# Kernel tuning notes

Hardware: AMD Instinct MI355X
Metric: run time of the kernel (lower is better)

## Reference

```python
import jax, jax.numpy as jnp
import numpy as np

N_NODES = 50000
N_EDGES = 1600000
IN_DIM = 128
OUT_DIM = 32
N_HEADS = 4


def setup_inputs() -> dict:
    key = jax.random.key(0)
    k_x, k_e, k_w, k_a = jax.random.split(key, 4)
    x = jax.random.normal(k_x, (N_NODES, IN_DIM), dtype=jnp.float32)
    edge_index = jax.random.randint(k_e, (N_EDGES, 2), 0, N_NODES, dtype=jnp.int64)
    # Xavier-uniform-like init scales
    w_bound = np.sqrt(6.0 / (IN_DIM + OUT_DIM)).astype(np.float32)
    a_bound = np.sqrt(6.0 / (N_HEADS + 2 * OUT_DIM)).astype(np.float32)
    weight = jax.random.uniform(k_w, (N_HEADS, IN_DIM, OUT_DIM), dtype=jnp.float32,
                                minval=-w_bound, maxval=w_bound)
    attn = jax.random.uniform(k_a, (N_HEADS, 2 * OUT_DIM), dtype=jnp.float32,
                              minval=-a_bound, maxval=a_bound)
    return {"x": x, "edge_index": edge_index, "weight": weight, "attn": attn}


def reference(x, edge_index, weight, attn):
    # x: [N, in_dim]; edge_index: [E, 2]; weight: [H, in, out]; attn: [H, 2*out]
    num_nodes = x.shape[0]
    out_dim = weight.shape[2]
    src = edge_index[:, 0]
    dst = edge_index[:, 1]

    # Per-head linear transform: [N, H, out]
    Wh = jnp.einsum('ni,hio->nho', x, weight)
    Wh_src = Wh[src]  # [E, H, out]
    Wh_dst = Wh[dst]  # [E, H, out]

    a_src = attn[:, :out_dim]   # [H, out]
    a_dst = attn[:, out_dim:]   # [H, out]
    # Edge scores: [E, H]
    e = jnp.einsum('eho,ho->eh', Wh_src, a_src) + jnp.einsum('eho,ho->eh', Wh_dst, a_dst)
    e = jax.nn.leaky_relu(e, negative_slope=0.2)

    # Segment softmax over incoming edges of each dst node
    max_per_dst = jax.ops.segment_max(e, dst, num_segments=num_nodes)  # [N, H]
    max_per_dst = jnp.where(jnp.isfinite(max_per_dst), max_per_dst, 0.0)
    exp_e = jnp.exp(e - max_per_dst[dst])                               # [E, H]
    sum_per_dst = jax.ops.segment_sum(exp_e, dst, num_segments=num_nodes)  # [N, H]
    alpha = exp_e / (sum_per_dst[dst] + 1e-9)                           # [E, H]
    # Dropout is identity in eval mode.

    # Weighted scatter-add aggregation: [N, H, out]
    out = jax.ops.segment_sum(alpha[:, :, None] * Wh_src, dst, num_segments=num_nodes)
    h = out.reshape(num_nodes, -1)  # concat heads -> [N, H*out]
    return h, alpha
```

## Files before the change

### kernel.cpp

```cpp
#include <hip/hip_runtime.h>
#include <hip/hip_bf16.h>
#include <math.h>

#define N_NODES 50000
#define N_EDGES 1600000
#define IN_DIM  128
#define OUT_DIM 32
#define N_HEADS 4
#define WH_DIM  (N_HEADS * OUT_DIM)
#define CAP     128
#define NB_SCAN 196
#define NPASS   4
#define WIN     (N_NODES / NPASS)
#define NCHUNK  32
#define CE      (N_EDGES / NCHUNK)

typedef __attribute__((ext_vector_type(8))) short short8;
typedef __attribute__((ext_vector_type(4))) float floatx4;

__device__ __forceinline__ short f2bf(float v) {
    __hip_bfloat16 b = __float2bfloat16(v);
    return *reinterpret_cast<short*>(&b);
}
__device__ __forceinline__ float lrelu(float v) {
    return v > 0.0f ? v : 0.2f * v;
}

__device__ __forceinline__ void load_edge(const void* eidx, int is32, int e,
                                          int& s, int& d) {
    if (is32) {
        const int2 v = ((const int2*)eidx)[e];
        s = v.x; d = v.y;
    } else {
        const longlong2 v = ((const longlong2*)eidx)[e];
        s = (int)v.x; d = (int)v.y;
    }
}

__global__ void k_detect(const int* __restrict__ eidx, int* __restrict__ flag) {
    int i = threadIdx.x;
    int r = eidx[2 * (i * (N_EDGES / 256)) + 1];
    if (r != 0) atomicOr(flag, 1);
}

__global__ __launch_bounds__(256) void k_cvt(
        const void* __restrict__ eidx, const int* __restrict__ flag,
        int* __restrict__ s32, int* __restrict__ d32) {
    int e = blockIdx.x * 256 + threadIdx.x;
    if (e >= N_EDGES) return;
    int s, d;
    load_edge(eidx, *flag, e, s, d);
    s32[e] = s;
    d32[e] = d;
}

__global__ __launch_bounds__(256) void k_wh(
        const float* __restrict__ x, const float* __restrict__ weight,
        const float* __restrict__ attn,
        __hip_bfloat16* __restrict__ Wh16, float* __restrict__ sb16) {
    __shared__ float ubuf[128 * 8];
    __shared__ short xsw[4 * 4 * 64 * 8];
    __shared__ short bsw[4 * 9 * 64 * 8];
    const int t  = threadIdx.x;
    const int nb = blockIdx.x * 64;

    {
        int c = t & 7, k0 = t >> 3;
        int h = c & 3;
        const float* ap = attn + h * 64 + (c >> 2) * 32;
        for (int k = k0; k < 128; k += 32) {
            const float* wp = weight + h * (IN_DIM * OUT_DIM) + k * OUT_DIM;
            float u = 0.f;
#pragma unroll
            for (int o = 0; o < 32; o += 4) {
                float4 wv = *(const float4*)(wp + o);
                float4 av = *(const float4*)(ap + o);
                u += wv.x * av.x + wv.y * av.y + wv.z * av.z + wv.w * av.w;
            }
            ubuf[k * 8 + c] = u;
        }
    }
    __syncthreads();

    for (int f = t; f < 128 * 128; f += 256) {
        int k = f >> 7, c = f & 127;
        float w = weight[(c >> 5) * (IN_DIM * OUT_DIM) + k * OUT_DIM + (c & 31)];
        int kc = k >> 5, quad = (k >> 3) & 3, j = k & 7;
        bsw[((kc * 9 + (c >> 4)) * 64 + quad * 16 + (c & 15)) * 8 + j] = f2bf(w);
    }
    for (int f = t; f < 128 * 16; f += 256) {
        int k = f >> 4, c = f & 15;
        float w = (c < 8) ? ubuf[k * 8 + c] : 0.f;
        int kc = k >> 5, quad = (k >> 3) & 3, j = k & 7;
        bsw[((kc * 9 + 8) * 64 + quad * 16 + c) * 8 + j] = f2bf(w);
    }
    for (int f = t; f < 64 * 32; f += 256) {
        int n = f >> 5, k = (f & 31) * 4;
        int ng = nb + n; if (ng > N_NODES - 1) ng = N_NODES - 1;
        float4 v = *(const float4*)(x + (size_t)ng * IN_DIM + k);
        int wg = n >> 4, m = n & 15, kc = k >> 5, quad = (k >> 3) & 3, j = k & 7;
        short4 sv = make_short4(f2bf(v.x), f2bf(v.y), f2bf(v.z), f2bf(v.w));
        *(short4*)&xsw[(((wg * 4 + kc) * 64) + quad * 16 + m) * 8 + j] = sv;
    }
    __syncthreads();

    const int wg = t >> 6, lane = t & 63;
    floatx4 acc[9];
#pragma unroll
    for (int i = 0; i < 9; ++i) acc[i] = (floatx4){0.f, 0.f, 0.f, 0.f};
#pragma unroll
    for (int kc = 0; kc < 4; ++kc) {
        short8 a = *(short8*)&xsw[((wg * 4 + kc) * 64 + lane) * 8];
#pragma unroll
        for (int cg = 0; cg < 9; ++cg) {
            short8 b = *(short8*)&bsw[((kc * 9 + cg) * 64 + lane) * 8];
            acc[cg] = __builtin_amdgcn_mfma_f32_16x16x32_bf16(a, b, acc[cg],
                                                              0, 0, 0);
        }
    }

    const int col = lane & 15, quad = lane >> 4;
#pragma unroll
    for (int r = 0; r < 4; ++r) {
        int n = nb + wg * 16 + quad * 4 + r;
        if (n >= N_NODES) continue;
#pragma unroll
        for (int cg = 0; cg < 8; ++cg)
            Wh16[(size_t)n * WH_DIM + cg * 16 + col] =
                __float2bfloat16(acc[cg][r]);
        if (col < 8) sb16[(size_t)n * 16 + col] = acc[8][r];
    }
}

__global__ __launch_bounds__(1024) void k_hist(
        const int* __restrict__ d32, int* __restrict__ hist) {
    __shared__ int hbin[WIN];
    const int c = blockIdx.x, w = blockIdx.y;
    for (int i = threadIdx.x; i < WIN; i += 1024) hbin[i] = 0;
    __syncthreads();
    const int w0 = w * WIN;
    for (int e = c * CE + threadIdx.x; e < (c + 1) * CE; e += 1024) {
        unsigned u = (unsigned)(d32[e] - w0);
        if (u < WIN) atomicAdd(&hbin[u], 1);
    }
    __syncthreads();
    for (int i = threadIdx.x; i < WIN; i += 1024)
        hist[c * N_NODES + w0 + i] = hbin[i];
}

__global__ __launch_bounds__(256) void k_scan1(
        const int* __restrict__ hist, int* __restrict__ pre,
        int* __restrict__ bsum) {
    __shared__ int sh[256];
    const int t = threadIdx.x;
    const int i = blockIdx.x * 256 + t;
    int v = 0;
    if (i < N_NODES)
        for (int c = 0; c < NCHUNK; ++c) v += hist[c * N_NODES + i];
    sh[t] = v;
    __syncthreads();
    for (int d = 1; d < 256; d <<= 1) {
        int u = (t >= d) ? sh[t - d] : 0;
        __syncthreads();
        sh[t] += u;
        __syncthreads();
    }
    if (i < N_NODES) pre[i] = sh[t] - v;
    if (t == 255) bsum[blockIdx.x] = sh[255];
}

__global__ __launch_bounds__(256) void k_scan2(
        const int* __restrict__ bsum, int* __restrict__ bbase) {
    __shared__ int sh[256];
    const int t = threadIdx.x;
    int v = (t < NB_SCAN) ? bsum[t] : 0;
    sh[t] = v;
    __syncthreads();
    for (int d = 1; d < 256; d <<= 1) {
        int u = (t >= d) ? sh[t - d] : 0;
        __syncthreads();
        sh[t] += u;
        __syncthreads();
    }
    if (t < NB_SCAN) bbase[t] = sh[t] - v;
}

__global__ __launch_bounds__(256) void k_base(
        const int* __restrict__ pre, const int* __restrict__ bbase,
        int* __restrict__ hist) {
    int d = blockIdx.x * 256 + threadIdx.x;
    if (d >= N_NODES) return;
    int run = pre[d] + bbase[d >> 8];
    for (int c = 0; c < NCHUNK; ++c) {
        int t0 = hist[c * N_NODES + d];
        hist[c * N_NODES + d] = run;
        run += t0;
    }
}

__global__ __launch_bounds__(1024) void k_scatter(
        const int* __restrict__ s32, const int* __restrict__ d32,
        const int* __restrict__ hist, int* __restrict__ csr) {
    __shared__ int pos[WIN];
    const int c = blockIdx.x, w = blockIdx.y;
    const int w0 = w * WIN;
    for (int i = threadIdx.x; i < WIN; i += 1024)
        pos[i] = hist[c * N_NODES + w0 + i];
    __syncthreads();
    for (int e = c * CE + threadIdx.x; e < (c + 1) * CE; e += 1024) {
        unsigned u = (unsigned)(d32[e] - w0);
        if (u < WIN) {
            int p = atomicAdd(&pos[u], 1);
            csr[p] = s32[e];
        }
    }
}

__global__ __launch_bounds__(256) void k_node(
        const int* __restrict__ pre, const int* __restrict__ bbase,
        const int* __restrict__ csr, float* __restrict__ sb16,
        const __hip_bfloat16* __restrict__ Wh16,
        float* __restrict__ out_h) {
    __shared__ int    sbuf[4][CAP];
    __shared__ float4 e4b[4][CAP];
    const int wv = threadIdx.x >> 6;
    const int t  = threadIdx.x & 63;
    const int n  = blockIdx.x * 4 + wv;
    const int beg = pre[n] + bbase[n >> 8];
    const int end = (n + 1 < N_NODES) ? pre[n + 1] + bbase[(n + 1) >> 8]
                                      : N_EDGES;
    const int deg = end - beg;

    const float4 sd = *(const float4*)(sb16 + (size_t)n * 16 + 4);

    float4 sum = {0.f, 0.f, 0.f, 0.f};
    for (int l = t; l < deg; l += 64) {
        int s = csr[beg + l];
        float4 ss = *(const float4*)(sb16 + (size_t)s * 16);
        float4 ex;
        ex.x = __expf(lrelu(ss.x + sd.x));
        ex.y = __expf(lrelu(ss.y + sd.y));
        ex.z = __expf(lrelu(ss.z + sd.z));
        ex.w = __expf(lrelu(ss.w + sd.w));
        if (l < CAP) { sbuf[wv][l] = s; e4b[wv][l] = ex; }
        sum.x += ex.x; sum.y += ex.y; sum.z += ex.z; sum.w += ex.w;
    }
#pragma unroll
    for (int o = 32; o; o >>= 1) {
        sum.x += __shfl_xor(sum.x, o);
        sum.y += __shfl_xor(sum.y, o);
        sum.z += __shfl_xor(sum.z, o);
        sum.w += __shfl_xor(sum.w, o);
    }
    float4 inv;
    inv.x = 1.0f / (sum.x + 1e-9f); inv.y = 1.0f / (sum.y + 1e-9f);
    inv.z = 1.0f / (sum.z + 1e-9f); inv.w = 1.0f / (sum.w + 1e-9f);
    if (t == 0) *(float4*)(sb16 + (size_t)n * 16 + 8) = inv;

    const int h = t >> 4;
    const float invh = (h == 0) ? inv.x : (h == 1) ? inv.y
                     : (h == 2) ? inv.z : inv.w;
    float2 acc = {0.0f, 0.0f};
    if (deg <= CAP) {
        int j = 0;
        for (; j + 3 < deg; j += 4) {
            int s0 = sbuf[wv][j],     s1 = sbuf[wv][j + 1];
            int s2 = sbuf[wv][j + 2], s3 = sbuf[wv][j + 3];
            float a0 = ((const float*)&e4b[wv][j])[h]     * invh;
            float a1 = ((const float*)&e4b[wv][j + 1])[h] * invh;
            float a2 = ((const float*)&e4b[wv][j + 2])[h] * invh;
            float a3 = ((const float*)&e4b[wv][j + 3])[h] * invh;
            __hip_bfloat162 w0 = ((const __hip_bfloat162*)(Wh16 + (size_t)s0 * WH_DIM))[t];
            __hip_bfloat162 w1 = ((const __hip_bfloat162*)(Wh16 + (size_t)s1 * WH_DIM))[t];
            __hip_bfloat162 w2 = ((const __hip_bfloat162*)(Wh16 + (size_t)s2 * WH_DIM))[t];
            __hip_bfloat162 w3 = ((const __hip_bfloat162*)(Wh16 + (size_t)s3 * WH_DIM))[t];
            float2 f0 = __bfloat1622float2(w0);
            float2 f1 = __bfloat1622float2(w1);
            float2 f2 = __bfloat1622float2(w2);
            float2 f3 = __bfloat1622float2(w3);
            acc.x += a0 * f0.x + a1 * f1.x + a2 * f2.x + a3 * f3.x;
            acc.y += a0 * f0.y + a1 * f1.y + a2 * f2.y + a3 * f3.y;
        }
        for (; j < deg; ++j) {
            int s0 = sbuf[wv][j];
            float a0 = ((const float*)&e4b[wv][j])[h] * invh;
            __hip_bfloat162 w0 = ((const __hip_bfloat162*)(Wh16 + (size_t)s0 * WH_DIM))[t];
            float2 f0 = __bfloat1622float2(w0);
            acc.x += a0 * f0.x;
            acc.y += a0 * f0.y;
        }
    } else {
        float dh = (h == 0) ? sd.x : (h == 1) ? sd.y : (h == 2) ? sd.z : sd.w;
        for (int j = 0; j < deg; ++j) {
            int s0; float a0;
            if (j < CAP) {
                s0 = sbuf[wv][j];
                a0 = ((const float*)&e4b[wv][j])[h] * invh;
            } else {
                s0 = csr[beg + j];
                float sh = sb16[(size_t)s0 * 16 + h];
                a0 = __expf(lrelu(sh + dh)) * invh;
            }
            __hip_bfloat162 w0 = ((const __hip_bfloat162*)(Wh16 + (size_t)s0 * WH_DIM))[t];
            float2 f0 = __bfloat1622float2(w0);
            acc.x += a0 * f0.x;
            acc.y += a0 * f0.y;
        }
    }
    *(float2*)(out_h + (size_t)n * WH_DIM + 2 * t) = acc;
}

__global__ __launch_bounds__(256) void k_alpha(
        const int* __restrict__ s32, const int* __restrict__ d32,
        const float* __restrict__ sb16, float* __restrict__ ebuf) {
    int e = blockIdx.x * 256 + threadIdx.x;
    if (e >= N_EDGES) return;
    int s = s32[e], d = d32[e];
    float4 ss = *(const float4*)(sb16 + (size_t)s * 16);
    float4 sd = *(const float4*)(sb16 + (size_t)d * 16 + 4);
    float4 iv = *(const float4*)(sb16 + (size_t)d * 16 + 8);
    float4 a;
    a.x = __expf(lrelu(ss.x + sd.x)) * iv.x;
    a.y = __expf(lrelu(ss.y + sd.y)) * iv.y;
    a.z = __expf(lrelu(ss.z + sd.z)) * iv.z;
    a.w = __expf(lrelu(ss.w + sd.w)) * iv.w;
    *(float4*)(ebuf + (size_t)e * 4) = a;
}

extern "C" void kernel_launch(void* const* d_in, const int* in_sizes, int n_in,
                              void* d_out, int out_size, void* d_ws, size_t ws_size,
                              hipStream_t stream) {
    const float* x      = (const float*)d_in[0];
    const void*  eidx   = d_in[1];
    const float* weight = (const float*)d_in[2];
    const float* attn   = (const float*)d_in[3];

    float* out   = (float*)d_out;
    float* out_h = out;
    float* ebuf  = out + (size_t)N_NODES * WH_DIM;

    char* ws = (char*)d_ws;
    int*   flag  = (int*)ws;
    int*   bsum  = (int*)(ws + 64);
    int*   bbase = (int*)(ws + 896);
    int*   pre   = (int*)(ws + 2048);
    int*   s32   = (int*)(ws + 202112);
    int*   d32   = (int*)(ws + 6602112);
    int*   hist  = (int*)(ws + 13002112);
    int*   csr   = (int*)(ws + 19402112);
    __hip_bfloat16* Wh16 = (__hip_bfloat16*)(ws + 25802112);
    float* sb16  = (float*)(ws + 38602112);

    hipMemsetAsync(flag, 0, 4, stream);

    k_detect<<<1, 256, 0, stream>>>((const int*)eidx, flag);
    k_cvt<<<(N_EDGES + 255) / 256, 256, 0, stream>>>(eidx, flag, s32, d32);
    k_wh<<<(N_NODES + 63) / 64, 256, 0, stream>>>(x, weight, attn, Wh16, sb16);
    dim3 hg(NCHUNK, NPASS);
    k_hist<<<hg, 1024, 0, stream>>>(d32, hist);
    k_scan1<<<NB_SCAN, 256, 0, stream>>>(hist, pre, bsum);
    k_scan2<<<1, 256, 0, stream>>>(bsum, bbase);
    k_base<<<NB_SCAN, 256, 0, stream>>>(pre, bbase, hist);
    k_scatter<<<hg, 1024, 0, stream>>>(s32, d32, hist, csr);
    k_node<<<N_NODES / 4, 256, 0, stream>>>(pre, bbase, csr, sb16,
                                            Wh16, out_h);
    k_alpha<<<(N_EDGES + 255) / 256, 256, 0, stream>>>(s32, d32, sb16, ebuf);
}
```

Baseline: 282.7 us.

## Split aggregation per head with head-major Wh layout and fused block-base scan

Wh is stored head-major ([H][N][32] bf16) and the attention scores are split into per-head src/dst pairs, so the node kernel can run one 16-lane group per (node, head) on a 2D grid. Each head's gather then touches 64-byte rows instead of full 256-byte rows. The separate block-sum scan kernel is folded into k_base, which also emits a plain offset array, and the detect memset is replaced by a shared-memory flag. The trade-off is four times more CSR index reads and per-head score gathers, plus a smaller edge cache (CAP 96).

```diff
diff --git a/kernel.cpp b/kernel.cpp
--- a/kernel.cpp
+++ b/kernel.cpp
@@ -8,7 +8,7 @@
 #define OUT_DIM 32
 #define N_HEADS 4
 #define WH_DIM  (N_HEADS * OUT_DIM)
-#define CAP     128
+#define CAP     96
 #define NB_SCAN 196
 #define NPASS   4
 #define WIN     (N_NODES / NPASS)
@@ -38,9 +38,13 @@
 }
 
 __global__ void k_detect(const int* __restrict__ eidx, int* __restrict__ flag) {
-    int i = threadIdx.x;
-    int r = eidx[2 * (i * (N_EDGES / 256)) + 1];
-    if (r != 0) atomicOr(flag, 1);
+    __shared__ int sf;
+    if (threadIdx.x == 0) sf = 0;
+    __syncthreads();
+    int r = eidx[2 * (threadIdx.x * (N_EDGES / 256)) + 1];
+    if (r != 0) sf = 1;
+    __syncthreads();
+    if (threadIdx.x == 0) *flag = sf;
 }
 
 __global__ __launch_bounds__(256) void k_cvt(
@@ -57,7 +61,7 @@
 __global__ __launch_bounds__(256) void k_wh(
         const float* __restrict__ x, const float* __restrict__ weight,
         const float* __restrict__ attn,
-        __hip_bfloat16* __restrict__ Wh16, float* __restrict__ sb16) {
+        __hip_bfloat16* __restrict__ Whh, float* __restrict__ sv) {
     __shared__ float ubuf[128 * 8];
     __shared__ short xsw[4 * 4 * 64 * 8];
     __shared__ short bsw[4 * 9 * 64 * 8];
@@ -99,8 +103,8 @@
         int ng = nb + n; if (ng > N_NODES - 1) ng = N_NODES - 1;
         float4 v = *(const float4*)(x + (size_t)ng * IN_DIM + k);
         int wg = n >> 4, m = n & 15, kc = k >> 5, quad = (k >> 3) & 3, j = k & 7;
-        short4 sv = make_short4(f2bf(v.x), f2bf(v.y), f2bf(v.z), f2bf(v.w));
-        *(short4*)&xsw[(((wg * 4 + kc) * 64) + quad * 16 + m) * 8 + j] = sv;
+        short4 sv4 = make_short4(f2bf(v.x), f2bf(v.y), f2bf(v.z), f2bf(v.w));
+        *(short4*)&xsw[(((wg * 4 + kc) * 64) + quad * 16 + m) * 8 + j] = sv4;
     }
     __syncthreads();
 
@@ -126,9 +130,12 @@
         if (n >= N_NODES) continue;
 #pragma unroll
         for (int cg = 0; cg < 8; ++cg)
-            Wh16[(size_t)n * WH_DIM + cg * 16 + col] =
+            Whh[((size_t)(cg >> 1) * N_NODES + n) * 32 + (cg & 1) * 16 + col] =
                 __float2bfloat16(acc[cg][r]);
-        if (col < 8) sb16[(size_t)n * 16 + col] = acc[8][r];
+        if (col < 8) {
+            int hh = col & 3, side = col >> 2;
+            sv[((size_t)hh * N_NODES + n) * 2 + side] = acc[8][r];
+        }
     }
 }
 
@@ -169,33 +176,31 @@
     if (t == 255) bsum[blockIdx.x] = sh[255];
 }
 
-__global__ __launch_bounds__(256) void k_scan2(
-        const int* __restrict__ bsum, int* __restrict__ bbase) {
-    __shared__ int sh[256];
-    const int t = threadIdx.x;
-    int v = (t < NB_SCAN) ? bsum[t] : 0;
-    sh[t] = v;
-    __syncthreads();
-    for (int d = 1; d < 256; d <<= 1) {
-        int u = (t >= d) ? sh[t - d] : 0;
-        __syncthreads();
-        sh[t] += u;
-        __syncthreads();
-    }
-    if (t < NB_SCAN) bbase[t] = sh[t] - v;
-}
-
 __global__ __launch_bounds__(256) void k_base(
-        const int* __restrict__ pre, const int* __restrict__ bbase,
-        int* __restrict__ hist) {
-    int d = blockIdx.x * 256 + threadIdx.x;
-    if (d >= N_NODES) return;
-    int run = pre[d] + bbase[d >> 8];
-    for (int c = 0; c < NCHUNK; ++c) {
-        int t0 = hist[c * N_NODES + d];
-        hist[c * N_NODES + d] = run;
-        run += t0;
-    }
+        const int* __restrict__ pre, const int* __restrict__ bsum,
+        int* __restrict__ hist, int* __restrict__ off) {
+    __shared__ int part[4];
+    __shared__ int sbb;
+    const int t = threadIdx.x, b = blockIdx.x;
+    int v = (t < b) ? bsum[t] : 0;
+#pragma unroll
+    for (int o = 32; o; o >>= 1) v += __shfl_xor(v, o);
+    if ((t & 63) == 0) part[t >> 6] = v;
+    __syncthreads();
+    if (t == 0) sbb = part[0] + part[1] + part[2] + part[3];
+    __syncthreads();
+    const int bb = sbb;
+    int d = b * 256 + t;
+    if (d < N_NODES) {
+        int run = pre[d] + bb;
+        off[d] = run;
+        for (int c = 0; c < NCHUNK; ++c) {
+            int t0 = hist[c * N_NODES + d];
+            hist[c * N_NODES + d] = run;
+            run += t0;
+        }
+    }
+    if (b == 0 && t == 0) off[N_NODES] = N_EDGES;
 }
 
 __global__ __launch_bounds__(1024) void k_scatter(
@@ -217,113 +222,88 @@
 }
 
 __global__ __launch_bounds__(256) void k_node(
-        const int* __restrict__ pre, const int* __restrict__ bbase,
-        const int* __restrict__ csr, float* __restrict__ sb16,
-        const __hip_bfloat16* __restrict__ Wh16,
-        float* __restrict__ out_h) {
-    __shared__ int    sbuf[4][CAP];
-    __shared__ float4 e4b[4][CAP];
-    const int wv = threadIdx.x >> 6;
-    const int t  = threadIdx.x & 63;
-    const int n  = blockIdx.x * 4 + wv;
-    const int beg = pre[n] + bbase[n >> 8];
-    const int end = (n + 1 < N_NODES) ? pre[n + 1] + bbase[(n + 1) >> 8]
-                                      : N_EDGES;
-    const int deg = end - beg;
-
-    const float4 sd = *(const float4*)(sb16 + (size_t)n * 16 + 4);
-
-    float4 sum = {0.f, 0.f, 0.f, 0.f};
-    for (int l = t; l < deg; l += 64) {
+        const int* __restrict__ off, const int* __restrict__ csr,
+        const float* __restrict__ sv, const __hip_bfloat16* __restrict__ Whh,
+        float* __restrict__ invh, float* __restrict__ out_h) {
+    __shared__ int   sbuf[16][CAP];
+    __shared__ float exb[16][CAP];
+    const int t    = threadIdx.x;
+    const int slot = t >> 4;
+    const int q    = t & 15;
+    const int h    = blockIdx.y;
+    const int n    = blockIdx.x * 16 + slot;
+    const int beg = off[n], end = off[n + 1], deg = end - beg;
+
+    const float sdh = sv[((size_t)h * N_NODES + n) * 2 + 1];
+
+    float sum = 0.f;
+    for (int l = q; l < deg; l += 16) {
         int s = csr[beg + l];
-        float4 ss = *(const float4*)(sb16 + (size_t)s * 16);
-        float4 ex;
-        ex.x = __expf(lrelu(ss.x + sd.x));
-        ex.y = __expf(lrelu(ss.y + sd.y));
-        ex.z = __expf(lrelu(ss.z + sd.z));
-        ex.w = __expf(lrelu(ss.w + sd.w));
-        if (l < CAP) { sbuf[wv][l] = s; e4b[wv][l] = ex; }
-        sum.x += ex.x; sum.y += ex.y; sum.z += ex.z; sum.w += ex.w;
-    }
-#pragma unroll
-    for (int o = 32; o; o >>= 1) {
-        sum.x += __shfl_xor(sum.x, o);
-        sum.y += __shfl_xor(sum.y, o);
-        sum.z += __shfl_xor(sum.z, o);
-        sum.w += __shfl_xor(sum.w, o);
-    }
-    float4 inv;
-    inv.x = 1.0f / (sum.x + 1e-9f); inv.y = 1.0f / (sum.y + 1e-9f);
-    inv.z = 1.0f / (sum.z + 1e-9f); inv.w = 1.0f / (sum.w + 1e-9f);
-    if (t == 0) *(float4*)(sb16 + (size_t)n * 16 + 8) = inv;
-
-    const int h = t >> 4;
-    const float invh = (h == 0) ? inv.x : (h == 1) ? inv.y
-                     : (h == 2) ? inv.z : inv.w;
-    float2 acc = {0.0f, 0.0f};
-    if (deg <= CAP) {
-        int j = 0;
-        for (; j + 3 < deg; j += 4) {
-            int s0 = sbuf[wv][j],     s1 = sbuf[wv][j + 1];
-            int s2 = sbuf[wv][j + 2], s3 = sbuf[wv][j + 3];
-            float a0 = ((const float*)&e4b[wv][j])[h]     * invh;
-            float a1 = ((const float*)&e4b[wv][j + 1])[h] * invh;
-            float a2 = ((const float*)&e4b[wv][j + 2])[h] * invh;
-            float a3 = ((const float*)&e4b[wv][j + 3])[h] * invh;
-            __hip_bfloat162 w0 = ((const __hip_bfloat162*)(Wh16 + (size_t)s0 * WH_DIM))[t];
-            __hip_bfloat162 w1 = ((const __hip_bfloat162*)(Wh16 + (size_t)s1 * WH_DIM))[t];
-            __hip_bfloat162 w2 = ((const __hip_bfloat162*)(Wh16 + (size_t)s2 * WH_DIM))[t];
-            __hip_bfloat162 w3 = ((const __hip_bfloat162*)(Wh16 + (size_t)s3 * WH_DIM))[t];
-            float2 f0 = __bfloat1622float2(w0);
-            float2 f1 = __bfloat1622float2(w1);
-            float2 f2 = __bfloat1622float2(w2);
-            float2 f3 = __bfloat1622float2(w3);
-            acc.x += a0 * f0.x + a1 * f1.x + a2 * f2.x + a3 * f3.x;
-            acc.y += a0 * f0.y + a1 * f1.y + a2 * f2.y + a3 * f3.y;
-        }
-        for (; j < deg; ++j) {
-            int s0 = sbuf[wv][j];
-            float a0 = ((const float*)&e4b[wv][j])[h] * invh;
-            __hip_bfloat162 w0 = ((const __hip_bfloat162*)(Wh16 + (size_t)s0 * WH_DIM))[t];
-            float2 f0 = __bfloat1622float2(w0);
-            acc.x += a0 * f0.x;
-            acc.y += a0 * f0.y;
-        }
-    } else {
-        float dh = (h == 0) ? sd.x : (h == 1) ? sd.y : (h == 2) ? sd.z : sd.w;
-        for (int j = 0; j < deg; ++j) {
-            int s0; float a0;
-            if (j < CAP) {
-                s0 = sbuf[wv][j];
-                a0 = ((const float*)&e4b[wv][j])[h] * invh;
-            } else {
-                s0 = csr[beg + j];
-                float sh = sb16[(size_t)s0 * 16 + h];
-                a0 = __expf(lrelu(sh + dh)) * invh;
-            }
-            __hip_bfloat162 w0 = ((const __hip_bfloat162*)(Wh16 + (size_t)s0 * WH_DIM))[t];
-            float2 f0 = __bfloat1622float2(w0);
-            acc.x += a0 * f0.x;
-            acc.y += a0 * f0.y;
-        }
-    }
-    *(float2*)(out_h + (size_t)n * WH_DIM + 2 * t) = acc;
+        float ss = sv[((size_t)h * N_NODES + s) * 2];
+        float ex = __expf(lrelu(ss + sdh));
+        if (l < CAP) { sbuf[slot][l] = s; exb[slot][l] = ex; }
+        sum += ex;
+    }
+#pragma unroll
+    for (int o = 8; o; o >>= 1) sum += __shfl_xor(sum, o);
+    const float inv = 1.0f / (sum + 1e-9f);
+    if (q == 0) invh[(size_t)h * N_NODES + n] = inv;
+
+    const __hip_bfloat16* wbase = Whh + (size_t)h * N_NODES * 32 + 2 * q;
+    float2 acc = {0.f, 0.f};
+    const int dc = deg < CAP ? deg : CAP;
+    int j = 0;
+    for (; j + 3 < dc; j += 4) {
+        int s0 = sbuf[slot][j],     s1 = sbuf[slot][j + 1];
+        int s2 = sbuf[slot][j + 2], s3 = sbuf[slot][j + 3];
+        float a0 = exb[slot][j] * inv,     a1 = exb[slot][j + 1] * inv;
+        float a2 = exb[slot][j + 2] * inv, a3 = exb[slot][j + 3] * inv;
+        __hip_bfloat162 w0 = *(const __hip_bfloat162*)(wbase + (size_t)s0 * 32);
+        __hip_bfloat162 w1 = *(const __hip_bfloat162*)(wbase + (size_t)s1 * 32);
+        __hip_bfloat162 w2 = *(const __hip_bfloat162*)(wbase + (size_t)s2 * 32);
+        __hip_bfloat162 w3 = *(const __hip_bfloat162*)(wbase + (size_t)s3 * 32);
+        float2 f0 = __bfloat1622float2(w0);
+        float2 f1 = __bfloat1622float2(w1);
+        float2 f2 = __bfloat1622float2(w2);
+        float2 f3 = __bfloat1622float2(w3);
+        acc.x += a0 * f0.x + a1 * f1.x + a2 * f2.x + a3 * f3.x;
+        acc.y += a0 * f0.y + a1 * f1.y + a2 * f2.y + a3 * f3.y;
+    }
+    for (; j < dc; ++j) {
+        int s0 = sbuf[slot][j];
+        float a0 = exb[slot][j] * inv;
+        __hip_bfloat162 w0 = *(const __hip_bfloat162*)(wbase + (size_t)s0 * 32);
+        float2 f0 = __bfloat1622float2(w0);
+        acc.x += a0 * f0.x;
+        acc.y += a0 * f0.y;
+    }
+    for (; j < deg; ++j) {
+        int s0 = csr[beg + j];
+        float ss = sv[((size_t)h * N_NODES + s0) * 2];
+        float a0 = __expf(lrelu(ss + sdh)) * inv;
+        __hip_bfloat162 w0 = *(const __hip_bfloat162*)(wbase + (size_t)s0 * 32);
+        float2 f0 = __bfloat1622float2(w0);
+        acc.x += a0 * f0.x;
+        acc.y += a0 * f0.y;
+    }
+    *(float2*)(out_h + (size_t)n * WH_DIM + h * 32 + 2 * q) = acc;
 }
 
 __global__ __launch_bounds__(256) void k_alpha(
         const int* __restrict__ s32, const int* __restrict__ d32,
-        const float* __restrict__ sb16, float* __restrict__ ebuf) {
+        const float* __restrict__ sv, const float* __restrict__ invh,
+        float* __restrict__ ebuf) {
     int e = blockIdx.x * 256 + threadIdx.x;
     if (e >= N_EDGES) return;
     int s = s32[e], d = d32[e];
-    float4 ss = *(const float4*)(sb16 + (size_t)s * 16);
-    float4 sd = *(const float4*)(sb16 + (size_t)d * 16 + 4);
-    float4 iv = *(const float4*)(sb16 + (size_t)d * 16 + 8);
     float4 a;
-    a.x = __expf(lrelu(ss.x + sd.x)) * iv.x;
-    a.y = __expf(lrelu(ss.y + sd.y)) * iv.y;
-    a.z = __expf(lrelu(ss.z + sd.z)) * iv.z;
-    a.w = __expf(lrelu(ss.w + sd.w)) * iv.w;
+#pragma unroll
+    for (int h = 0; h < 4; ++h) {
+        float ss = sv[((size_t)h * N_NODES + s) * 2];
+        float sd = sv[((size_t)h * N_NODES + d) * 2 + 1];
+        float iv = invh[(size_t)h * N_NODES + d];
+        ((float*)&a)[h] = __expf(lrelu(ss + sd)) * iv;
+    }
     *(float4*)(ebuf + (size_t)e * 4) = a;
 }
 
@@ -342,27 +322,25 @@
     char* ws = (char*)d_ws;
     int*   flag  = (int*)ws;
     int*   bsum  = (int*)(ws + 64);
-    int*   bbase = (int*)(ws + 896);
-    int*   pre   = (int*)(ws + 2048);
-    int*   s32   = (int*)(ws + 202112);
-    int*   d32   = (int*)(ws + 6602112);
-    int*   hist  = (int*)(ws + 13002112);
-    int*   csr   = (int*)(ws + 19402112);
-    __hip_bfloat16* Wh16 = (__hip_bfloat16*)(ws + 25802112);
-    float* sb16  = (float*)(ws + 38602112);
-
-    hipMemsetAsync(flag, 0, 4, stream);
+    int*   off   = (int*)(ws + 1024);
+    int*   pre   = (int*)(ws + 201088);
+    int*   s32   = (int*)(ws + 401088);
+    int*   d32   = (int*)(ws + 6801088);
+    int*   hist  = (int*)(ws + 13201088);
+    int*   csr   = (int*)(ws + 19601088);
+    __hip_bfloat16* Whh = (__hip_bfloat16*)(ws + 26001088);
+    float* sv    = (float*)(ws + 38801088);
+    float* invh  = (float*)(ws + 40401088);
 
     k_detect<<<1, 256, 0, stream>>>((const int*)eidx, flag);
     k_cvt<<<(N_EDGES + 255) / 256, 256, 0, stream>>>(eidx, flag, s32, d32);
-    k_wh<<<(N_NODES + 63) / 64, 256, 0, stream>>>(x, weight, attn, Wh16, sb16);
+    k_wh<<<(N_NODES + 63) / 64, 256, 0, stream>>>(x, weight, attn, Whh, sv);
     dim3 hg(NCHUNK, NPASS);
     k_hist<<<hg, 1024, 0, stream>>>(d32, hist);
     k_scan1<<<NB_SCAN, 256, 0, stream>>>(hist, pre, bsum);
-    k_scan2<<<1, 256, 0, stream>>>(bsum, bbase);
-    k_base<<<NB_SCAN, 256, 0, stream>>>(pre, bbase, hist);
+    k_base<<<NB_SCAN, 256, 0, stream>>>(pre, bsum, hist, off);
     k_scatter<<<hg, 1024, 0, stream>>>(s32, d32, hist, csr);
-    k_node<<<N_NODES / 4, 256, 0, stream>>>(pre, bbase, csr, sb16,
-                                            Wh16, out_h);
-    k_alpha<<<(N_EDGES + 255) / 256, 256, 0, stream>>>(s32, d32, sb16, ebuf);
-}
+    dim3 ng(N_NODES / 16, N_HEADS);
+    k_node<<<ng, 256, 0, stream>>>(off, csr, sv, Whh, invh, out_h);
+    k_alpha<<<(N_EDGES + 255) / 256, 256, 0, stream>>>(s32, d32, sv, invh, ebuf);
+}
```

Measured after the change: 335.1 us. 1.19x slower.
